# Performance work log

Hardware: AMD Instinct MI355X
Metric: run time of the kernel (lower is better)

The kernel has to match this reference:

```python
import jax, jax.numpy as jnp
import numpy as np

B, T, D, H = 4, 2048, 1024, 16
DK = D // H

def setup_inputs() -> dict:
    key = jax.random.key(0)
    k1, k2, k3 = jax.random.split(key, 3)
    x = jax.random.normal(k1, (B, T, D), dtype=jnp.float32)
    # torch nn.Linear weight layout: (out_features, in_features); y = x @ W.T
    s = 1.0 / np.sqrt(D)
    W_qkv = jax.random.uniform(k2, (3 * D, D), dtype=jnp.float32, minval=-s, maxval=s)
    W_o = jax.random.uniform(k3, (D, D), dtype=jnp.float32, minval=-s, maxval=s)
    return {"x": x, "W_qkv": W_qkv, "W_o": W_o}

def reference(x, W_qkv, W_o):
    Bq, Tq, C = x.shape
    qkv = jnp.einsum('btd,ed->bte', x, W_qkv)           # (B,T,3D)
    q, k, v = jnp.split(qkv, 3, axis=-1)
    # (B,H,T,DK)
    q = q.reshape(Bq, Tq, H, DK).transpose(0, 2, 1, 3)
    k = k.reshape(Bq, Tq, H, DK).transpose(0, 2, 1, 3)
    v = v.reshape(Bq, Tq, H, DK).transpose(0, 2, 1, 3)
    scores = jnp.einsum('bhqd,bhkd->bhqk', q, k) / jnp.sqrt(jnp.float32(DK))
    causal = jnp.triu(jnp.full((Tq, Tq), -jnp.inf, dtype=scores.dtype), k=1)
    scores = scores + causal[None, None, :, :]
    attn = jax.nn.softmax(scores, axis=-1)
    out = jnp.einsum('bhqk,bhkd->bhqd', attn, v)
    out = out.transpose(0, 2, 1, 3).reshape(Bq, Tq, C)
    return jnp.einsum('btd,ed->bte', out, W_o)
```

## Files before the change

### kernel.cpp

```cpp
#include <hip/hip_runtime.h>

#define BATCH 4
#define SEQ   2048
#define DIM   1024
#define NH    16
#define DK    64
#define QSCALE 0.18033688011112042f

typedef __bf16 bf16x8 __attribute__((ext_vector_type(8)));
typedef float  f32x4  __attribute__((ext_vector_type(4)));
typedef short  s16x4  __attribute__((ext_vector_type(4)));
typedef short  s16x8  __attribute__((ext_vector_type(8)));

__device__ __forceinline__ short f2b(float f) {
    unsigned u = __float_as_uint(f);
    u += 0x7FFFu + ((u >> 16) & 1u);
    return (short)(u >> 16);
}

__device__ __forceinline__ bf16x8 ldb(const short* p) {
    s16x8 v = *(const s16x8*)p;
    return __builtin_bit_cast(bf16x8, v);
}

__device__ __forceinline__ void ld16(const void* g, void* l) {
    __builtin_amdgcn_global_load_lds(
        (__attribute__((address_space(1))) void*)(unsigned long long)g,
        (__attribute__((address_space(3))) void*)l, 16, 0, 0);
}

__global__ __launch_bounds__(256)
void cvt_all(const float* __restrict__ x, const float* __restrict__ wq,
             const float* __restrict__ wo,
             short* __restrict__ xb, short* __restrict__ wqb, short* __restrict__ wob)
{
    const int NX4 = (BATCH*SEQ*DIM) / 4;
    const int NQ4 = (3*DIM*DIM) / 4;
    const int NO4 = (DIM*DIM) / 4;
    const int total = NX4 + NQ4 + NO4;
    for (int u = blockIdx.x * blockDim.x + threadIdx.x; u < total;
         u += gridDim.x * blockDim.x) {
        const float* src; short* dst; int off;
        if (u < NX4)            { src = x;  dst = xb;  off = u; }
        else if (u < NX4 + NQ4) { src = wq; dst = wqb; off = u - NX4; }
        else                    { src = wo; dst = wob; off = u - NX4 - NQ4; }
        f32x4 v = *(const f32x4*)&src[(size_t)off * 4];
        s16x4 o;
        o[0] = f2b(v[0]); o[1] = f2b(v[1]); o[2] = f2b(v[2]); o[3] = f2b(v[3]);
        *(s16x4*)&dst[(size_t)off * 4] = o;
    }
}

template<bool QKV>
__global__ __launch_bounds__(256)
void gemm_bt(const short* __restrict__ A, const short* __restrict__ Bm,
             int M, int N, int K,
             short* __restrict__ C0, short* __restrict__ C1, short* __restrict__ C2,
             float* __restrict__ Cf)
{
    __shared__ short As[128 * 64];
    __shared__ short Bs[128 * 64];
    const int tid  = threadIdx.x;
    const int lane = tid & 63;
    const int lr   = lane & 15;
    const int lg   = lane >> 4;
    const int wid  = tid >> 6;
    const int wr   = wid >> 1, wc = wid & 1;
    const long row0 = (long)blockIdx.y * 128;
    const long col0 = (long)blockIdx.x * 128;

    f32x4 acc[4][4] = {};

    for (int k0 = 0; k0 < K; k0 += 64) {
        #pragma unroll
        for (int i = 0; i < 4; ++i) {
            int off = (i * 256 + tid) * 8;
            int r = off >> 6, c = off & 63;
            ld16(&A[(row0 + r) * (long)K + k0 + c], &As[off]);
        }
        #pragma unroll
        for (int i = 0; i < 4; ++i) {
            int off = (i * 256 + tid) * 8;
            int r = off >> 6, c = off & 63;
            ld16(&Bm[(col0 + r) * (long)K + k0 + c], &Bs[off]);
        }
        __syncthreads();
        #pragma unroll
        for (int ks = 0; ks < 2; ++ks) {
            bf16x8 af[4], bfr[4];
            #pragma unroll
            for (int m = 0; m < 4; ++m)
                af[m] = ldb(&As[(wr*64 + m*16 + lr)*64 + ks*32 + lg*8]);
            #pragma unroll
            for (int n = 0; n < 4; ++n)
                bfr[n] = ldb(&Bs[(wc*64 + n*16 + lr)*64 + ks*32 + lg*8]);
            #pragma unroll
            for (int m = 0; m < 4; ++m)
                #pragma unroll
                for (int n = 0; n < 4; ++n)
                    acc[m][n] = __builtin_amdgcn_mfma_f32_16x16x32_bf16(
                        af[m], bfr[n], acc[m][n], 0, 0, 0);
        }
        __syncthreads();
    }

    if (QKV) {
        #pragma unroll
        for (int n = 0; n < 4; ++n) {
            const int gn    = (int)col0 + wc*64 + n*16 + lr;
            const int which = gn >> 10;
            const int wi    = gn & 1023;
            const int h = wi >> 6, dk = wi & 63;
            #pragma unroll
            for (int m = 0; m < 4; ++m) {
                const int gm0 = (int)row0 + wr*64 + m*16 + lg*4;
                const int b = gm0 >> 11, t0 = gm0 & 2047;
                if (which == 2) {
                    s16x4 v4;
                    #pragma unroll
                    for (int r = 0; r < 4; ++r) v4[r] = f2b(acc[m][n][r]);
                    *(s16x4*)&C2[((long)((b*NH + h)*DK + dk)) * SEQ + t0] = v4;
                } else {
                    short* dst = (which == 0) ? C0 : C1;
                    const float sc = (which == 0) ? QSCALE : 1.0f;
                    #pragma unroll
                    for (int r = 0; r < 4; ++r)
                        dst[((long)((b*NH + h)*SEQ + t0 + r)) * DK + dk] =
                            f2b(acc[m][n][r] * sc);
                }
            }
        }
    } else {
        #pragma unroll
        for (int m = 0; m < 4; ++m)
            #pragma unroll
            for (int r = 0; r < 4; ++r) {
                const long gm = row0 + wr*64 + m*16 + lg*4 + r;
                #pragma unroll
                for (int n = 0; n < 4; ++n)
                    Cf[gm * N + col0 + wc*64 + n*16 + lr] = acc[m][n][r];
            }
    }
}

__global__ __launch_bounds__(256, 2)
void attn(const short* __restrict__ Qb, const short* __restrict__ Kb,
          const short* __restrict__ Vt, short* __restrict__ Ob)
{
    __shared__ short Pl[4][2][16 * 72];
    const int tid  = threadIdx.x;
    const int lane = tid & 63;
    const int lr   = lane & 15, lg = lane >> 4;
    const int wid  = tid >> 6;
    const int bh   = blockIdx.y;
    const int b    = bh >> 4, h = bh & 15;
    const int qbase = (15 - (int)blockIdx.x) * 128 + wid * 32;

    const short* Qh = Qb + (long)bh * (SEQ * DK);
    const short* Kh = Kb + (long)bh * (SEQ * DK);
    const short* Vh = Vt + (long)bh * (DK * SEQ);
    short* PwA = &Pl[wid][0][0];
    short* PwB = &Pl[wid][1][0];

    const bf16x8 qfA0 = ldb(&Qh[(qbase + lr) * DK + lg * 8]);
    const bf16x8 qfA1 = ldb(&Qh[(qbase + lr) * DK + 32 + lg * 8]);
    const bf16x8 qfB0 = ldb(&Qh[(qbase + 16 + lr) * DK + lg * 8]);
    const bf16x8 qfB1 = ldb(&Qh[(qbase + 16 + lr) * DK + 32 + lg * 8]);

    f32x4 oA[4] = {}, oB[4] = {};
    float mA = -1e30f, lA = 0.f, mB = -1e30f, lB = 0.f;

    const int ntiles = ((qbase + 31) >> 6) + 1;

    bf16x8 kreg[8];
    #pragma unroll
    for (int kt = 0; kt < 4; ++kt) {
        kreg[kt*2]   = ldb(&Kh[(kt*16 + lr) * DK + lg * 8]);
        kreg[kt*2+1] = ldb(&Kh[(kt*16 + lr) * DK + 32 + lg * 8]);
    }

    for (int t = 0; t < ntiles; ++t) {
        const int k0 = t << 6;
        f32x4 sA[4], sB[4];
        __builtin_amdgcn_s_setprio(1);
        #pragma unroll
        for (int kt = 0; kt < 4; ++kt) {
            f32x4 zA = {}, zB = {};
            zA = __builtin_amdgcn_mfma_f32_16x16x32_bf16(kreg[kt*2],   qfA0, zA, 0, 0, 0);
            sA[kt] = __builtin_amdgcn_mfma_f32_16x16x32_bf16(kreg[kt*2+1], qfA1, zA, 0, 0, 0);
            zB = __builtin_amdgcn_mfma_f32_16x16x32_bf16(kreg[kt*2],   qfB0, zB, 0, 0, 0);
            sB[kt] = __builtin_amdgcn_mfma_f32_16x16x32_bf16(kreg[kt*2+1], qfB1, zB, 0, 0, 0);
        }
        __builtin_amdgcn_s_setprio(0);
        bf16x8 vreg[8];
        #pragma unroll
        for (int n2 = 0; n2 < 4; ++n2) {
            vreg[n2*2]   = ldb(&Vh[(n2*16 + lr) * SEQ + k0 + lg*8]);
            vreg[n2*2+1] = ldb(&Vh[(n2*16 + lr) * SEQ + k0 + 32 + lg*8]);
        }
        if (t + 1 < ntiles) {
            #pragma unroll
            for (int kt = 0; kt < 4; ++kt) {
                kreg[kt*2]   = ldb(&Kh[(k0 + 64 + kt*16 + lr) * DK + lg*8]);
                kreg[kt*2+1] = ldb(&Kh[(k0 + 64 + kt*16 + lr) * DK + 32 + lg*8]);
            }
        }
        if (t == ntiles - 1) {
            #pragma unroll
            for (int kt = 0; kt < 4; ++kt)
                #pragma unroll
                for (int r = 0; r < 4; ++r) {
                    const int kk = k0 + kt*16 + lg*4 + r;
                    if (kk > qbase + lr)      sA[kt][r] = -1e30f;
                    if (kk > qbase + 16 + lr) sB[kt][r] = -1e30f;
                }
        }
        {
            float tm = sA[0][0];
            #pragma unroll
            for (int kt = 0; kt < 4; ++kt)
                #pragma unroll
                for (int r = 0; r < 4; ++r) tm = fmaxf(tm, sA[kt][r]);
            tm = fmaxf(tm, __shfl_xor(tm, 16));
            tm = fmaxf(tm, __shfl_xor(tm, 32));
            const float mnew = fmaxf(mA, tm);
            const float corr = exp2f(mA - mnew);
            mA = mnew;
            float rs = 0.f;
            #pragma unroll
            for (int kt = 0; kt < 4; ++kt) {
                s16x4 pk;
                #pragma unroll
                for (int r = 0; r < 4; ++r) {
                    const float p = exp2f(sA[kt][r] - mnew);
                    rs += p; pk[r] = f2b(p);
                }
                *(s16x4*)&PwA[lr*72 + kt*16 + lg*4] = pk;
            }
            rs += __shfl_xor(rs, 16);
            rs += __shfl_xor(rs, 32);
            lA = lA * corr + rs;
            #pragma unroll
            for (int n2 = 0; n2 < 4; ++n2) oA[n2] *= corr;
        }
        {
            float tm = sB[0][0];
            #pragma unroll
            for (int kt = 0; kt < 4; ++kt)
                #pragma unroll
                for (int r = 0; r < 4; ++r) tm = fmaxf(tm, sB[kt][r]);
            tm = fmaxf(tm, __shfl_xor(tm, 16));
            tm = fmaxf(tm, __shfl_xor(tm, 32));
            const float mnew = fmaxf(mB, tm);
            const float corr = exp2f(mB - mnew);
            mB = mnew;
            float rs = 0.f;
            #pragma unroll
            for (int kt = 0; kt < 4; ++kt) {
                s16x4 pk;
                #pragma unroll
                for (int r = 0; r < 4; ++r) {
                    const float p = exp2f(sB[kt][r] - mnew);
                    rs += p; pk[r] = f2b(p);
                }
                *(s16x4*)&PwB[lr*72 + kt*16 + lg*4] = pk;
            }
            rs += __shfl_xor(rs, 16);
            rs += __shfl_xor(rs, 32);
            lB = lB * corr + rs;
            #pragma unroll
            for (int n2 = 0; n2 < 4; ++n2) oB[n2] *= corr;
        }
        __builtin_amdgcn_sched_barrier(0);
        __builtin_amdgcn_s_waitcnt(0xC07F);
        __builtin_amdgcn_sched_barrier(0);
        const bf16x8 pfA0 = ldb(&PwA[lr*72 + lg*8]);
        const bf16x8 pfA1 = ldb(&PwA[lr*72 + 32 + lg*8]);
        const bf16x8 pfB0 = ldb(&PwB[lr*72 + lg*8]);
        const bf16x8 pfB1 = ldb(&PwB[lr*72 + 32 + lg*8]);
        __builtin_amdgcn_s_setprio(1);
        #pragma unroll
        for (int n2 = 0; n2 < 4; ++n2) {
            oA[n2] = __builtin_amdgcn_mfma_f32_16x16x32_bf16(vreg[n2*2],   pfA0, oA[n2], 0, 0, 0);
            oA[n2] = __builtin_amdgcn_mfma_f32_16x16x32_bf16(vreg[n2*2+1], pfA1, oA[n2], 0, 0, 0);
            oB[n2] = __builtin_amdgcn_mfma_f32_16x16x32_bf16(vreg[n2*2],   pfB0, oB[n2], 0, 0, 0);
            oB[n2] = __builtin_amdgcn_mfma_f32_16x16x32_bf16(vreg[n2*2+1], pfB1, oB[n2], 0, 0, 0);
        }
        __builtin_amdgcn_s_setprio(0);
    }

    const float invA = 1.0f / lA;
    const float invB = 1.0f / lB;
    const long orowA = ((long)(b * SEQ + qbase + lr)) * DIM + h * DK;
    const long orowB = ((long)(b * SEQ + qbase + 16 + lr)) * DIM + h * DK;
    #pragma unroll
    for (int n2 = 0; n2 < 4; ++n2) {
        s16x4 ovA, ovB;
        #pragma unroll
        for (int r = 0; r < 4; ++r) {
            ovA[r] = f2b(oA[n2][r] * invA);
            ovB[r] = f2b(oB[n2][r] * invB);
        }
        *(s16x4*)&Ob[orowA + n2*16 + lg*4] = ovA;
        *(s16x4*)&Ob[orowB + n2*16 + lg*4] = ovB;
    }
}

extern "C" void kernel_launch(void* const* d_in, const int* in_sizes, int n_in,
                              void* d_out, int out_size, void* d_ws, size_t ws_size,
                              hipStream_t stream) {
    const float *x = nullptr, *wqkv = nullptr, *wo = nullptr;
    for (int i = 0; i < n_in; ++i) {
        if      (in_sizes[i] == BATCH*SEQ*DIM) x    = (const float*)d_in[i];
        else if (in_sizes[i] == 3*DIM*DIM)     wqkv = (const float*)d_in[i];
        else if (in_sizes[i] == DIM*DIM)       wo   = (const float*)d_in[i];
    }
    float* out = (float*)d_out;

    char* ws = (char*)d_ws;
    short* Xb  = (short*)(ws);
    short* Wqb = (short*)(ws + (16u<<20));
    short* Wob = (short*)(ws + (22u<<20));
    short* Qb  = (short*)(ws + (24u<<20));
    short* Kb  = (short*)(ws + (40u<<20));
    short* Vt  = (short*)(ws + (56u<<20));
    short* Ob  = Xb;

    cvt_all<<<2048, 256, 0, stream>>>(x, wqkv, wo, Xb, Wqb, Wob);

    gemm_bt<true><<<dim3(3*DIM/128, BATCH*SEQ/128), 256, 0, stream>>>(
        Xb, Wqb, BATCH*SEQ, 3*DIM, DIM, Qb, Kb, Vt, nullptr);

    attn<<<dim3(SEQ/128, BATCH*NH), 256, 0, stream>>>(Qb, Kb, Vt, Ob);

    gemm_bt<false><<<dim3(DIM/128, BATCH*SEQ/128), 256, 0, stream>>>(
        Ob, Wob, BATCH*SEQ, DIM, DIM, nullptr, nullptr, nullptr, out);
}
```

Baseline: 426.8 us.

## Share K/V tiles across waves via double-buffered swizzled LDS staging

Replaces per-wave direct global loads of K and V fragments with block-cooperative async copies (ld16) into double-buffered, XOR-swizzled LDS tiles. All four waves then read their fragments from LDS, cutting redundant global traffic fourfold. Each iteration needs block barriers, and waves with no causal work for a tile still wait at them. Launch bounds are raised to 3 blocks per CU to recover occupancy despite the extra 32KB of LDS.

```diff
diff --git a/kernel.cpp b/kernel.cpp
--- a/kernel.cpp
+++ b/kernel.cpp
@@ -143,10 +143,12 @@
     }
 }
 
-__global__ __launch_bounds__(256, 2)
+__global__ __launch_bounds__(256, 3)
 void attn(const short* __restrict__ Qb, const short* __restrict__ Kb,
           const short* __restrict__ Vt, short* __restrict__ Ob)
 {
+    __shared__ short Ks[2][64 * 64];
+    __shared__ short Vs[2][64 * 64];
     __shared__ short Pl[4][2][16 * 72];
     const int tid  = threadIdx.x;
     const int lane = tid & 63;
@@ -154,7 +156,9 @@
     const int wid  = tid >> 6;
     const int bh   = blockIdx.y;
     const int b    = bh >> 4, h = bh & 15;
-    const int qbase = (15 - (int)blockIdx.x) * 128 + wid * 32;
+    const int qb0  = (15 - (int)blockIdx.x) * 128;
+    const int qbase = qb0 + wid * 32;
+    const int NT   = (qb0 >> 6) + 2;
 
     const short* Qh = Qb + (long)bh * (SEQ * DK);
     const short* Kh = Kb + (long)bh * (SEQ * DK);
@@ -170,123 +174,149 @@
     f32x4 oA[4] = {}, oB[4] = {};
     float mA = -1e30f, lA = 0.f, mB = -1e30f, lB = 0.f;
 
-    const int ntiles = ((qbase + 31) >> 6) + 1;
-
-    bf16x8 kreg[8];
-    #pragma unroll
-    for (int kt = 0; kt < 4; ++kt) {
-        kreg[kt*2]   = ldb(&Kh[(kt*16 + lr) * DK + lg * 8]);
-        kreg[kt*2+1] = ldb(&Kh[(kt*16 + lr) * DK + 32 + lg * 8]);
-    }
-
-    for (int t = 0; t < ntiles; ++t) {
+    #define STAGE(bufi, k0_)                                                  \
+        {                                                                     \
+            _Pragma("unroll")                                                 \
+            for (int i_ = 0; i_ < 2; ++i_) {                                  \
+                const int idx_ = i_ * 256 + tid;        \
+                const int row_ = idx_ >> 3;                                   \
+                const int sc_  = ((idx_ & 7) ^ (row_ & 7)) * 8;               \
+                ld16(&Kh[(k0_ + row_) * DK + sc_], &Ks[bufi][idx_ * 8]);      \
+                ld16(&Vh[row_ * SEQ + (k0_) + sc_], &Vs[bufi][idx_ * 8]);     \
+            }                                                                 \
+        }
+
+    STAGE(0, 0)
+    __builtin_amdgcn_s_waitcnt(0x0F70);
+    __builtin_amdgcn_sched_barrier(0);
+    __builtin_amdgcn_s_barrier();
+
+    int cur = 0;
+    for (int t = 0; t < NT; ++t) {
         const int k0 = t << 6;
-        f32x4 sA[4], sB[4];
-        __builtin_amdgcn_s_setprio(1);
-        #pragma unroll
-        for (int kt = 0; kt < 4; ++kt) {
-            f32x4 zA = {}, zB = {};
-            zA = __builtin_amdgcn_mfma_f32_16x16x32_bf16(kreg[kt*2],   qfA0, zA, 0, 0, 0);
-            sA[kt] = __builtin_amdgcn_mfma_f32_16x16x32_bf16(kreg[kt*2+1], qfA1, zA, 0, 0, 0);
-            zB = __builtin_amdgcn_mfma_f32_16x16x32_bf16(kreg[kt*2],   qfB0, zB, 0, 0, 0);
-            sB[kt] = __builtin_amdgcn_mfma_f32_16x16x32_bf16(kreg[kt*2+1], qfB1, zB, 0, 0, 0);
-        }
-        __builtin_amdgcn_s_setprio(0);
-        bf16x8 vreg[8];
-        #pragma unroll
-        for (int n2 = 0; n2 < 4; ++n2) {
-            vreg[n2*2]   = ldb(&Vh[(n2*16 + lr) * SEQ + k0 + lg*8]);
-            vreg[n2*2+1] = ldb(&Vh[(n2*16 + lr) * SEQ + k0 + 32 + lg*8]);
-        }
-        if (t + 1 < ntiles) {
+        if (t + 1 < NT) {
+            STAGE(cur ^ 1, k0 + 64)
+            __builtin_amdgcn_s_waitcnt(0x0F74);
+        } else {
+            __builtin_amdgcn_s_waitcnt(0x0F70);
+        }
+        __builtin_amdgcn_sched_barrier(0);
+        __builtin_amdgcn_s_barrier();
+        __builtin_amdgcn_sched_barrier(0);
+
+        if (k0 <= qbase + 31) {
+            const int rswz = lr & 7;
+            bf16x8 kf[4][2];
             #pragma unroll
             for (int kt = 0; kt < 4; ++kt) {
-                kreg[kt*2]   = ldb(&Kh[(k0 + 64 + kt*16 + lr) * DK + lg*8]);
-                kreg[kt*2+1] = ldb(&Kh[(k0 + 64 + kt*16 + lr) * DK + 32 + lg*8]);
-            }
-        }
-        if (t == ntiles - 1) {
-            #pragma unroll
-            for (int kt = 0; kt < 4; ++kt)
-                #pragma unroll
-                for (int r = 0; r < 4; ++r) {
-                    const int kk = k0 + kt*16 + lg*4 + r;
-                    if (kk > qbase + lr)      sA[kt][r] = -1e30f;
-                    if (kk > qbase + 16 + lr) sB[kt][r] = -1e30f;
+                const int row = kt * 16 + lr;
+                kf[kt][0] = ldb(&Ks[cur][row * 64 + ((lg)     ^ rswz) * 8]);
+                kf[kt][1] = ldb(&Ks[cur][row * 64 + ((4 + lg) ^ rswz) * 8]);
+            }
+            f32x4 sA[4], sB[4];
+            __builtin_amdgcn_s_setprio(1);
+            #pragma unroll
+            for (int kt = 0; kt < 4; ++kt) {
+                f32x4 zA = {}, zB = {};
+                zA = __builtin_amdgcn_mfma_f32_16x16x32_bf16(kf[kt][0], qfA0, zA, 0, 0, 0);
+                sA[kt] = __builtin_amdgcn_mfma_f32_16x16x32_bf16(kf[kt][1], qfA1, zA, 0, 0, 0);
+                zB = __builtin_amdgcn_mfma_f32_16x16x32_bf16(kf[kt][0], qfB0, zB, 0, 0, 0);
+                sB[kt] = __builtin_amdgcn_mfma_f32_16x16x32_bf16(kf[kt][1], qfB1, zB, 0, 0, 0);
+            }
+            __builtin_amdgcn_s_setprio(0);
+            bf16x8 vf[4][2];
+            #pragma unroll
+            for (int n2 = 0; n2 < 4; ++n2) {
+                const int row = n2 * 16 + lr;
+                vf[n2][0] = ldb(&Vs[cur][row * 64 + ((lg)     ^ rswz) * 8]);
+                vf[n2][1] = ldb(&Vs[cur][row * 64 + ((4 + lg) ^ rswz) * 8]);
+            }
+            if (k0 + 63 > qbase) {
+                #pragma unroll
+                for (int kt = 0; kt < 4; ++kt)
+                    #pragma unroll
+                    for (int r = 0; r < 4; ++r) {
+                        const int kk = k0 + kt * 16 + lg * 4 + r;
+                        if (kk > qbase + lr)      sA[kt][r] = -1e30f;
+                        if (kk > qbase + 16 + lr) sB[kt][r] = -1e30f;
+                    }
+            }
+            {
+                float tm = sA[0][0];
+                #pragma unroll
+                for (int kt = 0; kt < 4; ++kt)
+                    #pragma unroll
+                    for (int r = 0; r < 4; ++r) tm = fmaxf(tm, sA[kt][r]);
+                tm = fmaxf(tm, __shfl_xor(tm, 16));
+                tm = fmaxf(tm, __shfl_xor(tm, 32));
+                const float mnew = fmaxf(mA, tm);
+                const float corr = exp2f(mA - mnew);
+                mA = mnew;
+                float rs = 0.f;
+                #pragma unroll
+                for (int kt = 0; kt < 4; ++kt) {
+                    s16x4 pk;
+                    #pragma unroll
+                    for (int r = 0; r < 4; ++r) {
+                        const float p = exp2f(sA[kt][r] - mnew);
+                        rs += p; pk[r] = f2b(p);
+                    }
+                    *(s16x4*)&PwA[lr*72 + kt*16 + lg*4] = pk;
                 }
-        }
-        {
-            float tm = sA[0][0];
-            #pragma unroll
-            for (int kt = 0; kt < 4; ++kt)
-                #pragma unroll
-                for (int r = 0; r < 4; ++r) tm = fmaxf(tm, sA[kt][r]);
-            tm = fmaxf(tm, __shfl_xor(tm, 16));
-            tm = fmaxf(tm, __shfl_xor(tm, 32));
-            const float mnew = fmaxf(mA, tm);
-            const float corr = exp2f(mA - mnew);
-            mA = mnew;
-            float rs = 0.f;
-            #pragma unroll
-            for (int kt = 0; kt < 4; ++kt) {
-                s16x4 pk;
-                #pragma unroll
-                for (int r = 0; r < 4; ++r) {
-                    const float p = exp2f(sA[kt][r] - mnew);
-                    rs += p; pk[r] = f2b(p);
+                rs += __shfl_xor(rs, 16);
+                rs += __shfl_xor(rs, 32);
+                lA = lA * corr + rs;
+                #pragma unroll
+                for (int n2 = 0; n2 < 4; ++n2) oA[n2] *= corr;
+            }
+            {
+                float tm = sB[0][0];
+                #pragma unroll
+                for (int kt = 0; kt < 4; ++kt)
+                    #pragma unroll
+                    for (int r = 0; r < 4; ++r) tm = fmaxf(tm, sB[kt][r]);
+                tm = fmaxf(tm, __shfl_xor(tm, 16));
+                tm = fmaxf(tm, __shfl_xor(tm, 32));
+                const float mnew = fmaxf(mB, tm);
+                const float corr = exp2f(mB - mnew);
+                mB = mnew;
+                float rs = 0.f;
+                #pragma unroll
+                for (int kt = 0; kt < 4; ++kt) {
+                    s16x4 pk;
+                    #pragma unroll
+                    for (int r = 0; r < 4; ++r) {
+                        const float p = exp2f(sB[kt][r] - mnew);
+                        rs += p; pk[r] = f2b(p);
+                    }
+                    *(s16x4*)&PwB[lr*72 + kt*16 + lg*4] = pk;
                 }
-                *(s16x4*)&PwA[lr*72 + kt*16 + lg*4] = pk;
-            }
-            rs += __shfl_xor(rs, 16);
-            rs += __shfl_xor(rs, 32);
-            lA = lA * corr + rs;
-            #pragma unroll
-            for (int n2 = 0; n2 < 4; ++n2) oA[n2] *= corr;
-        }
-        {
-            float tm = sB[0][0];
-            #pragma unroll
-            for (int kt = 0; kt < 4; ++kt)
-                #pragma unroll
-                for (int r = 0; r < 4; ++r) tm = fmaxf(tm, sB[kt][r]);
-            tm = fmaxf(tm, __shfl_xor(tm, 16));
-            tm = fmaxf(tm, __shfl_xor(tm, 32));
-            const float mnew = fmaxf(mB, tm);
-            const float corr = exp2f(mB - mnew);
-            mB = mnew;
-            float rs = 0.f;
-            #pragma unroll
-            for (int kt = 0; kt < 4; ++kt) {
-                s16x4 pk;
-                #pragma unroll
-                for (int r = 0; r < 4; ++r) {
-                    const float p = exp2f(sB[kt][r] - mnew);
-                    rs += p; pk[r] = f2b(p);
-                }
-                *(s16x4*)&PwB[lr*72 + kt*16 + lg*4] = pk;
-            }
-            rs += __shfl_xor(rs, 16);
-            rs += __shfl_xor(rs, 32);
-            lB = lB * corr + rs;
-            #pragma unroll
-            for (int n2 = 0; n2 < 4; ++n2) oB[n2] *= corr;
-        }
-        __builtin_amdgcn_sched_barrier(0);
-        __builtin_amdgcn_s_waitcnt(0xC07F);
-        __builtin_amdgcn_sched_barrier(0);
-        const bf16x8 pfA0 = ldb(&PwA[lr*72 + lg*8]);
-        const bf16x8 pfA1 = ldb(&PwA[lr*72 + 32 + lg*8]);
-        const bf16x8 pfB0 = ldb(&PwB[lr*72 + lg*8]);
-        const bf16x8 pfB1 = ldb(&PwB[lr*72 + 32 + lg*8]);
-        __builtin_amdgcn_s_setprio(1);
-        #pragma unroll
-        for (int n2 = 0; n2 < 4; ++n2) {
-            oA[n2] = __builtin_amdgcn_mfma_f32_16x16x32_bf16(vreg[n2*2],   pfA0, oA[n2], 0, 0, 0);
-            oA[n2] = __builtin_amdgcn_mfma_f32_16x16x32_bf16(vreg[n2*2+1], pfA1, oA[n2], 0, 0, 0);
-            oB[n2] = __builtin_amdgcn_mfma_f32_16x16x32_bf16(vreg[n2*2],   pfB0, oB[n2], 0, 0, 0);
-            oB[n2] = __builtin_amdgcn_mfma_f32_16x16x32_bf16(vreg[n2*2+1], pfB1, oB[n2], 0, 0, 0);
-        }
-        __builtin_amdgcn_s_setprio(0);
+                rs += __shfl_xor(rs, 16);
+                rs += __shfl_xor(rs, 32);
+                lB = lB * corr + rs;
+                #pragma unroll
+                for (int n2 = 0; n2 < 4; ++n2) oB[n2] *= corr;
+            }
+            __builtin_amdgcn_sched_barrier(0);
+            __builtin_amdgcn_s_waitcnt(0xC07F);
+            __builtin_amdgcn_sched_barrier(0);
+            const bf16x8 pfA0 = ldb(&PwA[lr*72 + lg*8]);
+            const bf16x8 pfA1 = ldb(&PwA[lr*72 + 32 + lg*8]);
+            const bf16x8 pfB0 = ldb(&PwB[lr*72 + lg*8]);
+            const bf16x8 pfB1 = ldb(&PwB[lr*72 + 32 + lg*8]);
+            __builtin_amdgcn_s_setprio(1);
+            #pragma unroll
+            for (int n2 = 0; n2 < 4; ++n2) {
+                oA[n2] = __builtin_amdgcn_mfma_f32_16x16x32_bf16(vf[n2][0], pfA0, oA[n2], 0, 0, 0);
+                oA[n2] = __builtin_amdgcn_mfma_f32_16x16x32_bf16(vf[n2][1], pfA1, oA[n2], 0, 0, 0);
+                oB[n2] = __builtin_amdgcn_mfma_f32_16x16x32_bf16(vf[n2][0], pfB0, oB[n2], 0, 0, 0);
+                oB[n2] = __builtin_amdgcn_mfma_f32_16x16x32_bf16(vf[n2][1], pfB1, oB[n2], 0, 0, 0);
+            }
+            __builtin_amdgcn_s_setprio(0);
+        }
+
+        __builtin_amdgcn_s_barrier();
+        cur ^= 1;
     }
 
     const float invA = 1.0f / lA;
```

After: 353.6 us. -17.1%, faster.
